# Kernel optimization log

Measured on AMD Instinct MI355X. Metric: run time of the kernel, lower is better.

## Reference

```python
import jax, jax.numpy as jnp
import numpy as np
import math

N = 20000      # nodes
E = 150000     # edges
IN = 256       # in_dim
HID = 256      # n_hid / out_dim
T = 4          # num_types
R = 8          # num_relations
H = 8          # n_heads
DK = HID // H  # d_k = 32
L = 2          # n_layers
MAXLEN = 240   # RTE max_len


def _rte_table():
    # fixed sinusoid table from RelTemporalEncoding (requires_grad=False in torch)
    pos = np.arange(MAXLEN, dtype=np.float64)[:, None]
    div = np.exp(np.arange(0, HID, 2, dtype=np.float64) * -(math.log(10000.0) / HID))
    emb = np.zeros((MAXLEN, HID), dtype=np.float64)
    emb[:, 0::2] = np.sin(pos * div) / math.sqrt(HID)
    emb[:, 1::2] = np.cos(pos * div) / math.sqrt(HID)
    return jnp.asarray(emb, dtype=jnp.float32)


def setup_inputs() -> dict:
    key = jax.random.key(0)
    ks = jax.random.split(key, 20)
    node_feature = jax.random.normal(ks[0], (N, IN), jnp.float32)
    node_type = jax.random.randint(ks[1], (N,), 0, T)
    edge_index = jax.random.randint(ks[2], (2, E), 0, N)
    edge_type = jax.random.randint(ks[3], (E,), 0, R)
    edge_time = jax.random.randint(ks[4], (E,), 0, MAXLEN)

    s_in = 1.0 / math.sqrt(IN)
    s_h = 1.0 / math.sqrt(HID)
    s_g = math.sqrt(2.0 / (DK + DK))  # glorot for relation mats

    adapt_W = jax.random.normal(ks[5], (T, IN, HID), jnp.float32) * s_in
    adapt_b = jnp.zeros((T, HID), jnp.float32)
    k_W = jax.random.normal(ks[6], (L, T, HID, HID), jnp.float32) * s_h
    k_b = jnp.zeros((L, T, HID), jnp.float32)
    q_W = jax.random.normal(ks[7], (L, T, HID, HID), jnp.float32) * s_h
    q_b = jnp.zeros((L, T, HID), jnp.float32)
    v_W = jax.random.normal(ks[8], (L, T, HID, HID), jnp.float32) * s_h
    v_b = jnp.zeros((L, T, HID), jnp.float32)
    a_W = jax.random.normal(ks[9], (L, T, HID, HID), jnp.float32) * s_h
    a_b = jnp.zeros((L, T, HID), jnp.float32)
    rel_pri = jnp.ones((L, R, H), jnp.float32)
    rel_att = jax.random.normal(ks[10], (L, R, H, DK, DK), jnp.float32) * s_g
    rel_msg = jax.random.normal(ks[11], (L, R, H, DK, DK), jnp.float32) * s_g
    skip = jnp.ones((L, T), jnp.float32)
    rte_W = jax.random.normal(ks[12], (L, HID, HID), jnp.float32) * s_h
    rte_b = jnp.zeros((L, HID), jnp.float32)
    rte_emb = _rte_table()

    return dict(node_feature=node_feature, node_type=node_type, edge_time=edge_time,
                edge_index=edge_index, edge_type=edge_type,
                adapt_W=adapt_W, adapt_b=adapt_b, k_W=k_W, k_b=k_b, q_W=q_W, q_b=q_b,
                v_W=v_W, v_b=v_b, a_W=a_W, a_b=a_b, rel_pri=rel_pri, rel_att=rel_att,
                rel_msg=rel_msg, skip=skip, rte_W=rte_W, rte_b=rte_b, rte_emb=rte_emb)


def _typed_linear(x, W, b, types):
    # x: [M, din]; W: [T, din, dout]; per-row type-selected linear (T dense GEMMs + select)
    out = jnp.zeros((x.shape[0], W.shape[-1]), x.dtype)
    for t in range(T):
        out = jnp.where((types == t)[:, None], x @ W[t] + b[t], out)
    return out


def _hgt_forward(node_feature, node_type, edge_time, edge_index, edge_type,
                 adapt_W, adapt_b, k_W, k_b, q_W, q_b, v_W, v_b, a_W, a_b,
                 rel_pri, rel_att, rel_msg, skip, rte_W, rte_b, rte_emb):
    # adapt: per-type tanh(Linear) (dropout is identity at p=0)
    x = jnp.tanh(_typed_linear(node_feature, adapt_W, adapt_b, node_type))
    src, tgt = edge_index[0], edge_index[1]   # j (source), i (target)
    st, tt = node_type[src], node_type[tgt]
    sqrt_dk = math.sqrt(DK)
    att = None
    rte = rte_emb[edge_time]                  # [E, HID]
    for l in range(L):
        x_j = x[src] + (rte @ rte_W[l] + rte_b[l])   # RTE added to source repr
        x_i = x[tgt]
        q = _typed_linear(x_i, q_W[l], q_b[l], tt).reshape(E, H, DK)
        k = _typed_linear(x_j, k_W[l], k_b[l], st).reshape(E, H, DK)
        v = _typed_linear(x_j, v_W[l], v_b[l], st).reshape(E, H, DK)
        att_e = jnp.zeros((E, H), x.dtype)
        msg = jnp.zeros((E, H, DK), x.dtype)
        for r in range(R):
            kr = jnp.einsum('ehd,hdk->ehk', k, rel_att[l, r])
            vr = jnp.einsum('ehd,hdk->ehk', v, rel_msg[l, r])
            a = (q * kr).sum(-1) * rel_pri[l, r] / sqrt_dk
            m = edge_type == r
            att_e = jnp.where(m[:, None], a, att_e)
            msg = jnp.where(m[:, None, None], vr, msg)
        # segment softmax over target node ids
        amax = jax.ops.segment_max(att_e, tgt, num_segments=N)
        ex = jnp.exp(att_e - amax[tgt])
        denom = jax.ops.segment_sum(ex, tgt, num_segments=N)
        alpha = ex / denom[tgt]                       # [E, H]
        agg = jax.ops.segment_sum(msg * alpha[:, :, None], tgt, num_segments=N)
        agg = jax.nn.gelu(agg.reshape(N, HID), approximate=False)
        trans = _typed_linear(agg, a_W[l], a_b[l], node_type)
        sk = jax.nn.sigmoid(skip[l])[node_type][:, None]
        x = trans * sk + x * (1.0 - sk)               # no LayerNorm (use_norm=False)
        att = alpha
    return att, x


def reference(node_feature, node_type, edge_time, edge_index, edge_type,
              adapt_W, adapt_b, k_W, k_b, q_W, q_b, v_W, v_b, a_W, a_b,
              rel_pri, rel_att, rel_msg, skip, rte_W, rte_b, rte_emb):
    return _hgt_forward(node_feature, node_type, edge_time, edge_index, edge_type,
                        adapt_W, adapt_b, k_W, k_b, q_W, q_b, v_W, v_b, a_W, a_b,
                        rel_pri, rel_att, rel_msg, skip, rte_W, rte_b, rte_emb)
```

## Files before the change

### kernel.cpp

```cpp
#include <hip/hip_runtime.h>
#include <hip/hip_fp16.h>

#define NN    20000
#define NE    150000
#define HD    256
#define NT    4
#define NR    8
#define NH    8
#define DKq   32
#define NL    2
#define MAXL  240
#define HBLK  256
#define SCB   ((NN + 255)/256)
#define TMAX  632
#define FOLDC 15
#define FTR   64
#define INV_SQRT_DK 0.17677669529663687f

typedef _Float16 f16x4 __attribute__((ext_vector_type(4)));
typedef _Float16 f16x8 __attribute__((ext_vector_type(8)));
typedef float    f32x4v __attribute__((ext_vector_type(4)));

__global__ __launch_bounds__(256) void k_nhist(const int* __restrict__ ntype, int* __restrict__ nhist)
{
    __shared__ int h[NT];
    const int tid = threadIdx.x, b = blockIdx.x;
    if (tid < NT) h[tid] = 0;
    __syncthreads();
    const int cn = (NN + HBLK-1)/HBLK;
    const int nEnd = min((b+1)*cn, NN);
    for (int i = b*cn + tid; i < nEnd; i += 256) atomicAdd(&h[ntype[i]], 1);
    __syncthreads();
    if (tid < NT) nhist[b*NT + tid] = h[tid];
}
__global__ void k_nscan(const int* __restrict__ nhist, int* __restrict__ noff, int* __restrict__ nbase,
                        int* __restrict__ tlist, int* __restrict__ tcount)
{
    __shared__ int tot[NT];
    const int tid = threadIdx.x;
    if (tid < NT){
        int s = 0;
        for (int b = 0; b < HBLK; b++) s += nhist[b*NT + tid];
        tot[tid] = s;
    }
    __syncthreads();
    if (tid == 0){ noff[0]=0; for (int t=0;t<NT;t++) noff[t+1]=noff[t]+tot[t]; }
    if (tid < NT){
        int base = 0; for (int t=0;t<tid;t++) base += tot[t];
        int run = 0;
        for (int b=0;b<HBLK;b++){ nbase[b*NT+tid] = base + run; run += nhist[b*NT+tid]; }
    }
    __syncthreads();
    if (tid == 0){
        int c = 0;
        for (int t = 0; t < NT; t++){
            const int ntile = (tot[t] + 31) >> 5;
            for (int rt = 0; rt < ntile; rt++) tlist[c++] = (t << 20) | rt;
        }
        *tcount = c;
    }
}
__global__ __launch_bounds__(256) void k_nscatter(const int* __restrict__ ntype,
    const int* __restrict__ nbase, int* __restrict__ nbucket)
{
    __shared__ int cur[NT];
    const int tid = threadIdx.x, b = blockIdx.x;
    if (tid < NT) cur[tid] = nbase[b*NT + tid];
    __syncthreads();
    const int cn = (NN + HBLK-1)/HBLK;
    const int nEnd = min((b+1)*cn, NN);
    for (int i = b*cn + tid; i < nEnd; i += 256)
        nbucket[atomicAdd(&cur[ntype[i]], 1)] = i;
}

__global__ void k_zero_bins(int* __restrict__ cnt){
    int i = blockIdx.x*256 + threadIdx.x;
    if (i < NN) cnt[i] = 0;
}
__global__ void k_csr_hist(const int* __restrict__ ei, int* __restrict__ cnt){
    int e = blockIdx.x*256 + threadIdx.x;
    if (e >= NE) return;
    atomicAdd(&cnt[ei[NE+e]], 1);
}
__global__ __launch_bounds__(256) void k_scan1(const int* __restrict__ cnt,
    int* __restrict__ tgt_off, int* __restrict__ bsum)
{
    __shared__ int sh[256];
    const int t = threadIdx.x, b = blockIdx.x;
    const int i = b*256 + t;
    const int v = (i < NN) ? cnt[i] : 0;
    sh[t] = v;
    __syncthreads();
    #pragma unroll
    for (int d = 1; d < 256; d <<= 1){
        const int u = (t >= d) ? sh[t-d] : 0;
        __syncthreads();
        sh[t] += u;
        __syncthreads();
    }
    if (i < NN) tgt_off[i] = sh[t] - v;
    if (t == 255) bsum[b] = sh[255];
}
__global__ __launch_bounds__(128) void k_scan2(const int* __restrict__ bsum,
    int* __restrict__ bbase, int* __restrict__ tgt_off)
{
    __shared__ int sh[128];
    const int t = threadIdx.x;
    const int v = (t < SCB) ? bsum[t] : 0;
    sh[t] = v;
    __syncthreads();
    #pragma unroll
    for (int d = 1; d < 128; d <<= 1){
        const int u = (t >= d) ? sh[t-d] : 0;
        __syncthreads();
        sh[t] += u;
        __syncthreads();
    }
    if (t < SCB) bbase[t] = sh[t] - v;
    if (t == 0) tgt_off[NN] = NE;
}
__global__ __launch_bounds__(256) void k_scan3(int* __restrict__ tgt_off,
    const int* __restrict__ bbase, int* __restrict__ binCur)
{
    const int i = blockIdx.x*256 + threadIdx.x;
    if (i >= NN) return;
    const int o = tgt_off[i] + bbase[blockIdx.x];
    tgt_off[i] = o;
    binCur[i] = o;
}
__global__ void k_csr_scatter(const int* __restrict__ ei, const int* __restrict__ etype,
    const int* __restrict__ etime, const int* __restrict__ ntype,
    int* __restrict__ binCur, int* __restrict__ src_s, int* __restrict__ combo_s,
    int* __restrict__ eid_s)
{
    int e = blockIdx.x*256 + threadIdx.x;
    if (e >= NE) return;
    const int tgt = ei[NE+e], r = etype[e], src = ei[e];
    const int pos = atomicAdd(&binCur[tgt], 1);
    src_s[pos] = src;
    combo_s[pos] = (etime[e]*NT + ntype[src]) | (r << 12);
    eid_s[pos] = e;
}
__global__ void k_tgtmap(const int* __restrict__ tgt_off, int* __restrict__ tgt_srt)
{
    const int n = blockIdx.x*256 + threadIdx.x;
    if (n >= NN) return;
    const int e0 = tgt_off[n], e1 = tgt_off[n+1];
    for (int j = e0; j < e1; j++) tgt_srt[j] = n;
}

__global__ __launch_bounds__(256) void k_w2f16_big(
    const float* __restrict__ adaptW, const float* __restrict__ qW, const float* __restrict__ kW,
    const float* __restrict__ vW, const float* __restrict__ aW, _Float16* __restrict__ out)
{
    const int y = blockIdx.y;
    const float* src; int m;
    if (y < 4){ src = adaptW; m = y; }
    else if (y < 12){ src = qW; m = y-4; }
    else if (y < 20){ src = kW; m = y-12; }
    else if (y < 28){ src = vW; m = y-20; }
    else { src = aW; m = y-28; }
    const float* ip = src + (size_t)m*65536;
    _Float16* op = out + (size_t)y*65536;
    const int tid4 = blockIdx.x*256 + threadIdx.x;
    const int k4 = tid4 >> 8, c = tid4 & 255;
    f16x4 hv;
    #pragma unroll
    for (int j = 0; j < 4; j++)
        hv[j] = (_Float16)ip[(size_t)(((k4*4 + j) << 8) + c)];
    *reinterpret_cast<f16x4*>(&op[(size_t)tid4 * 4]) = hv;
}
__global__ __launch_bounds__(256) void k_w2f16_rel(
    const float* __restrict__ attW, const float* __restrict__ msgW, _Float16* __restrict__ out)
{
    const int y = blockIdx.y;
    const float* ip = (y < 128) ? (attW + (size_t)y*1024) : (msgW + (size_t)(y-128)*1024);
    _Float16* op = out + (size_t)y*1024;
    const int tid4 = threadIdx.x;
    const int k4 = tid4 >> 5, c = tid4 & 31;
    f16x4 hv;
    #pragma unroll
    for (int j = 0; j < 4; j++)
        hv[j] = (_Float16)ip[(size_t)(((k4*4 + j) << 5) + c)];
    *reinterpret_cast<f16x4*>(&op[(size_t)tid4 * 4]) = hv;
}

__global__ __launch_bounds__(256) void k_x(
    const float* __restrict__ inF, const _Float16* __restrict__ inH,
    const _Float16* __restrict__ Wb, const float* __restrict__ bb, void* __restrict__ out,
    const int* __restrict__ nbucket, const int* __restrict__ noff,
    const int* __restrict__ tlist, const int* __restrict__ tcount,
    int mode, int oh, const float* __restrict__ skipv, const _Float16* __restrict__ xoldH)
{
    if ((int)blockIdx.x >= *tcount) return;
    const int ent = tlist[blockIdx.x];
    const int t = ent >> 20, rowTile = ent & 0xFFFFF;
    const int start = noff[t], cnt = noff[t+1] - start;

    const int tid = threadIdx.x;
    const int w = tid >> 6, lane = tid & 63;
    const int lrow = lane & 15, lgrp = lane >> 4;

    __shared__ _Float16 Al[32][260];
    __shared__ int nid[32];

    if (tid < 32){
        const int gr = rowTile*32 + tid;
        nid[tid] = (gr < cnt) ? nbucket[start + gr] : -1;
    }
    __syncthreads();
    {
        const int r = tid >> 3;
        const int arow = nid[r];
        if (inH){
            const _Float16* ap = (arow >= 0) ? (inH + (size_t)arow*HD) : nullptr;
            #pragma unroll
            for (int j = 0; j < 8; j++){
                const int f4 = (tid & 7) + j*8;
                f16x4 hv = {0,0,0,0};
                if (ap) hv = *reinterpret_cast<const f16x4*>(ap + f4*4);
                *reinterpret_cast<f16x4*>(&Al[r][f4*4]) = hv;
            }
        } else {
            const float* ap = (arow >= 0) ? (inF + (size_t)arow*HD) : nullptr;
            #pragma unroll
            for (int j = 0; j < 8; j++){
                const int f4 = (tid & 7) + j*8;
                float4 v = make_float4(0.f,0.f,0.f,0.f);
                if (ap) v = *reinterpret_cast<const float4*>(ap + f4*4);
                f16x4 hv;
                hv[0]=(_Float16)v.x; hv[1]=(_Float16)v.y; hv[2]=(_Float16)v.z; hv[3]=(_Float16)v.w;
                *reinterpret_cast<f16x4*>(&Al[r][f4*4]) = hv;
            }
        }
    }
    __syncthreads();

    float sk = 0.f;
    if (mode == 2) sk = 1.f/(1.f + __expf(-skipv[t]));

    const _Float16* W = Wb + (size_t)t*HD*HD;
    const float* bias = bb + (size_t)t*HD;
    f32x4v acc[4][2];
    #pragma unroll
    for (int cs = 0; cs < 4; cs++){
        acc[cs][0] = (f32x4v){0.f,0.f,0.f,0.f};
        acc[cs][1] = (f32x4v){0.f,0.f,0.f,0.f};
    }
    #pragma unroll 4
    for (int kc = 0; kc < 16; kc++){
        f16x4 bf[4];
        #pragma unroll
        for (int cs = 0; cs < 4; cs++)
            bf[cs] = *reinterpret_cast<const f16x4*>(
                &W[(size_t)((kc*4 + lgrp)*HD + w*64 + cs*16 + lrow)*4]);
        const f16x4 af0 = *reinterpret_cast<const f16x4*>(&Al[lrow][kc*16 + lgrp*4]);
        const f16x4 af1 = *reinterpret_cast<const f16x4*>(&Al[16 + lrow][kc*16 + lgrp*4]);
        #pragma unroll
        for (int cs = 0; cs < 4; cs++){
            acc[cs][0] = __builtin_amdgcn_mfma_f32_16x16x16f16(af0, bf[cs], acc[cs][0], 0,0,0);
            acc[cs][1] = __builtin_amdgcn_mfma_f32_16x16x16f16(af1, bf[cs], acc[cs][1], 0,0,0);
        }
    }
    #pragma unroll
    for (int cs = 0; cs < 4; cs++){
        const int col = w*64 + cs*16 + lrow;
        const float bcol = bias[col];
        #pragma unroll
        for (int rt = 0; rt < 2; rt++){
            #pragma unroll
            for (int i = 0; i < 4; i++){
                const int lr = rt*16 + lgrp*4 + i;
                const int gr = rowTile*32 + lr;
                if (gr >= cnt) continue;
                const int node = nid[lr];
                float v = acc[cs][rt][i] + bcol;
                if (mode == 1) v = tanhf(v);
                else if (mode == 2){
                    const float xo = (float)xoldH[(size_t)node*HD + col];
                    v = v*sk + xo*(1.f - sk);
                }
                if (oh) ((_Float16*)out)[(size_t)node*HD + col] = (_Float16)v;
                else    ((float*)out)[(size_t)node*HD + col] = v;
            }
        }
    }
}

__global__ __launch_bounds__(256) void k_qkv(
    const _Float16* __restrict__ xh,
    const _Float16* __restrict__ Wq, const float* __restrict__ bq, _Float16* __restrict__ oq,
    const _Float16* __restrict__ Wk, const float* __restrict__ bk, _Float16* __restrict__ okk,
    const _Float16* __restrict__ Wv, const float* __restrict__ bv, _Float16* __restrict__ ov,
    const int* __restrict__ nbucket, const int* __restrict__ noff,
    const int* __restrict__ tlist, const int* __restrict__ tcount)
{
    if ((int)blockIdx.x >= *tcount) return;
    const int ent = tlist[blockIdx.x];
    const int t = ent >> 20, rowTile = ent & 0xFFFFF;
    const int start = noff[t], cnt = noff[t+1] - start;
    const int sel = blockIdx.y;
    const _Float16* Wb = (sel==0 ? Wq : (sel==1 ? Wk : Wv));
    const float* bb = (sel==0 ? bq : (sel==1 ? bk : bv));
    _Float16* out = (sel==0 ? oq : (sel==1 ? okk : ov));

    const int tid = threadIdx.x;
    const int w = tid >> 6, lane = tid & 63;
    const int lrow = lane & 15, lgrp = lane >> 4;

    __shared__ _Float16 Al[32][260];
    __shared__ __align__(16) _Float16 Ol[32][264];
    __shared__ int nid[32];

    if (tid < 32){
        const int gr = rowTile*32 + tid;
        nid[tid] = (gr < cnt) ? nbucket[start + gr] : -1;
    }
    __syncthreads();
    {
        const int r = tid >> 3;
        const int arow = nid[r];
        const _Float16* ap = (arow >= 0) ? (xh + (size_t)arow*HD) : nullptr;
        #pragma unroll
        for (int j = 0; j < 8; j++){
            const int f4 = (tid & 7) + j*8;
            f16x4 hv = {0,0,0,0};
            if (ap) hv = *reinterpret_cast<const f16x4*>(ap + f4*4);
            *reinterpret_cast<f16x4*>(&Al[r][f4*4]) = hv;
        }
    }
    __syncthreads();

    const _Float16* W = Wb + (size_t)t*HD*HD;
    const float* bias = bb + (size_t)t*HD;
    f32x4v acc[4][2];
    #pragma unroll
    for (int cs = 0; cs < 4; cs++){
        acc[cs][0] = (f32x4v){0.f,0.f,0.f,0.f};
        acc[cs][1] = (f32x4v){0.f,0.f,0.f,0.f};
    }
    #pragma unroll 4
    for (int kc = 0; kc < 16; kc++){
        f16x4 bf[4];
        #pragma unroll
        for (int cs = 0; cs < 4; cs++)
            bf[cs] = *reinterpret_cast<const f16x4*>(
                &W[(size_t)((kc*4 + lgrp)*HD + w*64 + cs*16 + lrow)*4]);
        const f16x4 af0 = *reinterpret_cast<const f16x4*>(&Al[lrow][kc*16 + lgrp*4]);
        const f16x4 af1 = *reinterpret_cast<const f16x4*>(&Al[16 + lrow][kc*16 + lgrp*4]);
        #pragma unroll
        for (int cs = 0; cs < 4; cs++){
            acc[cs][0] = __builtin_amdgcn_mfma_f32_16x16x16f16(af0, bf[cs], acc[cs][0], 0,0,0);
            acc[cs][1] = __builtin_amdgcn_mfma_f32_16x16x16f16(af1, bf[cs], acc[cs][1], 0,0,0);
        }
    }
    #pragma unroll
    for (int cs = 0; cs < 4; cs++){
        const int col = w*64 + cs*16 + lrow;
        const float bcol = bias[col];
        #pragma unroll
        for (int rt = 0; rt < 2; rt++){
            #pragma unroll
            for (int i = 0; i < 4; i++){
                const int lr = rt*16 + lgrp*4 + i;
                Ol[lr][col] = (_Float16)(acc[cs][rt][i] + bcol);
            }
        }
    }
    __syncthreads();
    {
        const int fcb = tid & 31;
        #pragma unroll
        for (int it = 0; it < 4; it++){
            const int rr = (tid >> 5) + it*8;
            const int node = nid[rr];
            if (node < 0) continue;
            const f16x8 v = *reinterpret_cast<const f16x8*>(&Ol[rr][fcb*8]);
            *reinterpret_cast<f16x8*>(&out[(size_t)node*HD + fcb*8]) = v;
        }
    }
}

__global__ __launch_bounds__(256) void k_row_gemm(
    const float* __restrict__ A, const float* __restrict__ W, const float* __restrict__ bias,
    float* __restrict__ C)
{
    const int row = blockIdx.x, d = threadIdx.x;
    __shared__ float ar[HD];
    ar[d] = A[(size_t)row*HD + d];
    __syncthreads();
    float acc = bias[d];
    #pragma unroll 8
    for (int k=0;k<HD;k++) acc = fmaf(ar[k], W[(size_t)k*HD + d], acc);
    C[(size_t)row*HD + d] = acc;
}
__global__ __launch_bounds__(256) void k_row_gemm2(
    const float* __restrict__ A, const float* __restrict__ kWb, const float* __restrict__ vWb,
    _Float16* __restrict__ Kc, _Float16* __restrict__ Vc)
{
    const int row = blockIdx.x, ty = blockIdx.y, d = threadIdx.x;
    const float* W = ((blockIdx.z == 0) ? kWb : vWb) + (size_t)ty*HD*HD;
    _Float16* C = (blockIdx.z == 0) ? Kc : Vc;
    __shared__ float ar[HD];
    ar[d] = A[(size_t)row*HD + d];
    __syncthreads();
    float acc = 0.f;
    #pragma unroll 8
    for (int k=0;k<HD;k++) acc = fmaf(ar[k], W[(size_t)k*HD + d], acc);
    C[(size_t)row*(NT*HD) + ty*HD + d] = (_Float16)acc;
}

__global__ __launch_bounds__(256) void k_fold2(
    const _Float16* __restrict__ INa, const _Float16* __restrict__ MATa, _Float16* __restrict__ OUTa,
    const _Float16* __restrict__ INb, const _Float16* __restrict__ MATb, _Float16* __restrict__ OUTb,
    int M, int nbx)
{
    const int r = blockIdx.y;
    const _Float16* IN = blockIdx.z ? INb : INa;
    const _Float16* MATF = blockIdx.z ? MATb : MATa;
    _Float16* OUT = blockIdx.z ? OUTb : OUTa;
    const int lane = threadIdx.x & 63, w = threadIdx.x >> 6;
    const int lrow = lane & 15, lgrp = lane >> 4;
    f16x4 b[NH][2][2];
    const _Float16* Mr = MATF + (size_t)r*NH*1024;
    #pragma unroll
    for (int h = 0; h < NH; h++)
      #pragma unroll
      for (int kb = 0; kb < 2; kb++)
        #pragma unroll
        for (int hf = 0; hf < 2; hf++)
            b[h][kb][hf] = *reinterpret_cast<const f16x4*>(
                &Mr[(size_t)h*1024 + (size_t)(((kb*4 + lgrp)*32) + hf*16 + lrow)*4]);
    const int ntiles = M >> 4;
    for (int t = (int)blockIdx.x*4 + w; t < ntiles; t += nbx*4){
        const int row0 = t*16;
        const _Float16* inrow = IN + (size_t)(row0 + lrow)*HD;
        f16x4 a[NH][2];
        #pragma unroll
        for (int h = 0; h < NH; h++)
          #pragma unroll
          for (int kb = 0; kb < 2; kb++)
              a[h][kb] = *reinterpret_cast<const f16x4*>(&inrow[h*32 + kb*16 + lgrp*4]);
        #pragma unroll
        for (int h = 0; h < NH; h++){
          #pragma unroll
          for (int hf = 0; hf < 2; hf++){
              f32x4v acc = {0.f,0.f,0.f,0.f};
              acc = __builtin_amdgcn_mfma_f32_16x16x16f16(a[h][0], b[h][0][hf], acc, 0,0,0);
              acc = __builtin_amdgcn_mfma_f32_16x16x16f16(a[h][1], b[h][1][hf], acc, 0,0,0);
              #pragma unroll
              for (int i = 0; i < 4; i++){
                  const int rr = lgrp*4 + i;
                  OUT[((size_t)(row0+rr)*NR + r)*HD + h*32 + hf*16 + lrow] = (_Float16)acc[i];
              }
          }
        }
    }
}

__global__ __launch_bounds__(256) void k_fold2x(
    const _Float16* __restrict__ INa, const _Float16* __restrict__ MATa, _Float16* __restrict__ OUTa,
    const _Float16* __restrict__ INb, const _Float16* __restrict__ MATb, _Float16* __restrict__ OUTb)
{
    const int bid = blockIdx.x;
    const int xcd = bid & 7;
    const int s = bid >> 3;
    const int tr = xcd*8 + (s >> 4);
    const int item = s & 15;
    const int r = item & 7;
    const _Float16* IN = (item >> 3) ? INb : INa;
    const _Float16* MATF = (item >> 3) ? MATb : MATa;
    _Float16* OUT = (item >> 3) ? OUTb : OUTa;

    const int lane = threadIdx.x & 63, w = threadIdx.x >> 6;
    const int lrow = lane & 15, lgrp = lane >> 4;

    __shared__ __align__(16) _Float16 tile[4][16][264];

    f16x4 b[NH][2][2];
    const _Float16* Mr = MATF + (size_t)r*NH*1024;
    #pragma unroll
    for (int h = 0; h < NH; h++)
      #pragma unroll
      for (int kb = 0; kb < 2; kb++)
        #pragma unroll
        for (int hf = 0; hf < 2; hf++)
            b[h][kb][hf] = *reinterpret_cast<const f16x4*>(
                &Mr[(size_t)h*1024 + (size_t)(((kb*4 + lgrp)*32) + hf*16 + lrow)*4]);

    const int frow = lane >> 5;
    const int fcb  = lane & 31;
    const int ntiles = NN >> 4;
    for (int t = tr*4 + w; t < ntiles; t += FTR*4){
        const int row0 = t*16;
        const _Float16* inrow = IN + (size_t)(row0 + lrow)*HD;
        f16x4 a[NH][2];
        #pragma unroll
        for (int h = 0; h < NH; h++)
          #pragma unroll
          for (int kb = 0; kb < 2; kb++)
              a[h][kb] = *reinterpret_cast<const f16x4*>(&inrow[h*32 + kb*16 + lgrp*4]);
        #pragma unroll
        for (int h = 0; h < NH; h++){
          #pragma unroll
          for (int hf = 0; hf < 2; hf++){
              f32x4v acc = {0.f,0.f,0.f,0.f};
              acc = __builtin_amdgcn_mfma_f32_16x16x16f16(a[h][0], b[h][0][hf], acc, 0,0,0);
              acc = __builtin_amdgcn_mfma_f32_16x16x16f16(a[h][1], b[h][1][hf], acc, 0,0,0);
              const int col = h*32 + hf*16 + lrow;
              #pragma unroll
              for (int i = 0; i < 4; i++)
                  tile[w][lgrp*4 + i][col] = (_Float16)acc[i];
          }
        }
        asm volatile("s_waitcnt lgkmcnt(0)" ::: "memory");
        __builtin_amdgcn_sched_barrier(0);
        #pragma unroll
        for (int jj = 0; jj < 8; jj++){
            const int rr = jj*2 + frow;
            const f16x8 v = *reinterpret_cast<const f16x8*>(&tile[w][rr][fcb*8]);
            *reinterpret_cast<f16x8*>(&OUT[((size_t)(row0+rr)*NR + r)*HD + fcb*8]) = v;
        }
        asm volatile("s_waitcnt lgkmcnt(0)" ::: "memory");
        __builtin_amdgcn_sched_barrier(0);
    }
}

__global__ __launch_bounds__(256) void k_edge(
    const _Float16* __restrict__ q0, const _Float16* __restrict__ kA, const _Float16* __restrict__ KcA,
    const _Float16* __restrict__ vM, const _Float16* __restrict__ VcM,
    const float* __restrict__ relP,
    const int* __restrict__ tgt_off, const int* __restrict__ src_s, const int* __restrict__ combo_s,
    _Float16* __restrict__ agg,
    float* __restrict__ s_arr, float* __restrict__ mbuf, float* __restrict__ lbuf, int store_s)
{
    const int n = blockIdx.x*4 + (threadIdx.x >> 6);
    if (n >= NN) return;
    const int lane = threadIdx.x & 63;
    const int h = lane >> 3, c4 = (lane & 7) << 2;
    const int col = h*32 + c4;
    const int e0 = tgt_off[n], e1 = tgt_off[n+1];

    const f16x4 qh = *reinterpret_cast<const f16x4*>(&q0[(size_t)n*HD + col]);
    const float q0v = (float)qh[0], q1v = (float)qh[1], q2v = (float)qh[2], q3v = (float)qh[3];
    float m = -INFINITY, l = 0.f;
    float a0=0.f, a1=0.f, a2=0.f, a3=0.f;

    if (e0 < e1){
        int cwA = combo_s[e0];
        const int srcA0 = src_s[e0];
        const int rA0 = cwA >> 12, comboA0 = cwA & 0xFFF;
        f16x4 kaA = *reinterpret_cast<const f16x4*>(&kA [((size_t)srcA0*NR + rA0)*HD + col]);
        f16x4 kcA = *reinterpret_cast<const f16x4*>(&KcA[((size_t)comboA0*NR + rA0)*HD + col]);
        f16x4 vmA = *reinterpret_cast<const f16x4*>(&vM [((size_t)srcA0*NR + rA0)*HD + col]);
        f16x4 vcA = *reinterpret_cast<const f16x4*>(&VcM[((size_t)comboA0*NR + rA0)*HD + col]);
        const int j1 = min(e0+1, e1-1);
        int srcB = src_s[j1], cwB = combo_s[j1];

        for (int j = e0; j < e1; j++){
            const int rB = cwB >> 12, comboB = cwB & 0xFFF;
            const size_t offSB = ((size_t)srcB*NR + rB)*HD + col;
            const size_t offCB = ((size_t)comboB*NR + rB)*HD + col;
            const f16x4 kaN = *reinterpret_cast<const f16x4*>(&kA [offSB]);
            const f16x4 kcN = *reinterpret_cast<const f16x4*>(&KcA[offCB]);
            const f16x4 vmN = *reinterpret_cast<const f16x4*>(&vM [offSB]);
            const f16x4 vcN = *reinterpret_cast<const f16x4*>(&VcM[offCB]);
            const int jn = min(j+2, e1-1);
            const int srcN = src_s[jn], cwN = combo_s[jn];

            const int r = cwA >> 12;
            float s = q0v*((float)kaA[0]+(float)kcA[0])
                    + q1v*((float)kaA[1]+(float)kcA[1])
                    + q2v*((float)kaA[2]+(float)kcA[2])
                    + q3v*((float)kaA[3]+(float)kcA[3]);
            s += __shfl_xor(s, 1); s += __shfl_xor(s, 2); s += __shfl_xor(s, 4);
            s *= relP[r*NH + h] * INV_SQRT_DK;
            if (store_s && (lane & 7) == 0) s_arr[(size_t)j*NH + h] = s;
            const float mn = fmaxf(m, s);
            const float sc = __expf(m - mn);
            const float p  = __expf(s - mn);
            l = l*sc + p;
            m = mn;
            a0 = a0*sc + p*((float)vmA[0] + (float)vcA[0]);
            a1 = a1*sc + p*((float)vmA[1] + (float)vcA[1]);
            a2 = a2*sc + p*((float)vmA[2] + (float)vcA[2]);
            a3 = a3*sc + p*((float)vmA[3] + (float)vcA[3]);

            cwA = cwB;
            kaA = kaN; kcA = kcN; vmA = vmN; vcA = vcN;
            srcB = srcN; cwB = cwN;
        }
    }
    const float inv = (l > 0.f) ? 1.f/l : 0.f;
    a0 *= inv; a1 *= inv; a2 *= inv; a3 *= inv;
    f16x4 o;
    o[0] = (_Float16)(0.5f*a0*(1.f + erff(a0*0.70710678118654752f)));
    o[1] = (_Float16)(0.5f*a1*(1.f + erff(a1*0.70710678118654752f)));
    o[2] = (_Float16)(0.5f*a2*(1.f + erff(a2*0.70710678118654752f)));
    o[3] = (_Float16)(0.5f*a3*(1.f + erff(a3*0.70710678118654752f)));
    *reinterpret_cast<f16x4*>(&agg[(size_t)n*HD + col]) = o;
    if (store_s && (lane & 7) == 0){
        mbuf[(size_t)n*NH + h] = m;
        lbuf[(size_t)n*NH + h] = l;
    }
}

__global__ void k_alpha(const float* __restrict__ s_arr, const int* __restrict__ eid_s,
                        const float* __restrict__ mbuf, const float* __restrict__ lbuf,
                        const int* __restrict__ tgt_srt, float* __restrict__ out_att)
{
    int i = blockIdx.x*256 + threadIdx.x;
    if (i >= NE*NH) return;
    const int j = i >> 3, h = i & 7;
    const int t = tgt_srt[j];
    const float a = __expf(s_arr[i] - mbuf[(size_t)t*NH + h]) / lbuf[(size_t)t*NH + h];
    out_att[(size_t)eid_s[j]*NH + h] = a;
}

extern "C" void kernel_launch(void* const* d_in, const int* in_sizes, int n_in,
                              void* d_out, int out_size, void* d_ws, size_t ws_size,
                              hipStream_t stream)
{
    const float* node_feature = (const float*)d_in[0];
    const int*   node_type    = (const int*)d_in[1];
    const int*   edge_time    = (const int*)d_in[2];
    const int*   edge_index   = (const int*)d_in[3];
    const int*   edge_type    = (const int*)d_in[4];
    const float* adapt_W = (const float*)d_in[5];
    const float* adapt_b = (const float*)d_in[6];
    const float* k_W = (const float*)d_in[7];
    const float* k_b = (const float*)d_in[8];
    const float* q_W = (const float*)d_in[9];
    const float* q_b = (const float*)d_in[10];
    const float* v_W = (const float*)d_in[11];
    const float* v_b = (const float*)d_in[12];
    const float* a_W = (const float*)d_in[13];
    const float* a_b = (const float*)d_in[14];
    const float* rel_pri = (const float*)d_in[15];
    const float* rel_att = (const float*)d_in[16];
    const float* rel_msg = (const float*)d_in[17];
    const float* skip  = (const float*)d_in[18];
    const float* rte_W = (const float*)d_in[19];
    const float* rte_b = (const float*)d_in[20];
    const float* rte_emb = (const float*)d_in[21];

    char* wp = (char*)d_ws;
    auto alloc_f = [&](size_t n)->float*{ float* p=(float*)wp; wp += n*sizeof(float); return p; };
    auto alloc_i = [&](size_t n)->int*  { int*   p=(int*)wp;   wp += n*sizeof(int);   return p; };
    auto alloc_h = [&](size_t n)->_Float16*{ _Float16* p=(_Float16*)wp; wp += n*sizeof(_Float16); return p; };
    _Float16* xh0 = alloc_h((size_t)NN*HD);
    _Float16* xh1 = alloc_h((size_t)NN*HD);
    _Float16* q0h = alloc_h((size_t)NN*HD);
    _Float16* k0h = alloc_h((size_t)NN*HD);
    _Float16* v0h = alloc_h((size_t)NN*HD);
    _Float16* aggh= alloc_h((size_t)NN*HD);
    float* s_arr = alloc_f((size_t)NE*NH);
    float* mbuf  = alloc_f((size_t)NN*NH);
    float* lbuf  = alloc_f((size_t)NN*NH);
    float* rteP  = alloc_f((size_t)MAXL*HD);
    _Float16* Kch = alloc_h((size_t)MAXL*NT*HD);
    _Float16* Vch = alloc_h((size_t)MAXL*NT*HD);
    _Float16* kavm = alloc_h((size_t)NN*NR*HD);
    _Float16* vmh  = alloc_h((size_t)NN*NR*HD);
    _Float16* kcaA0 = alloc_h((size_t)MAXL*NT*NR*HD);
    _Float16* kcaA1 = alloc_h((size_t)MAXL*NT*NR*HD);
    _Float16* kcaM0 = alloc_h((size_t)MAXL*NT*NR*HD);
    _Float16* kcaM1 = alloc_h((size_t)MAXL*NT*NR*HD);
    _Float16* wF   = alloc_h((size_t)36*65536);
    _Float16* relF = alloc_h((size_t)256*1024);
    int* nbucket = alloc_i(NN);
    int* nhist   = alloc_i(HBLK*NT);
    int* nbase   = alloc_i(HBLK*NT);
    int* noff    = alloc_i(8);
    int* tlist   = alloc_i(TMAX);
    int* tcount  = alloc_i(8);
    int* cnt     = alloc_i(NN);
    int* bsum    = alloc_i(SCB);
    int* bbase   = alloc_i(SCB);
    int* binCur  = alloc_i(NN);
    int* tgt_off = alloc_i(NN+1);
    int* src_s   = alloc_i(NE);
    int* combo_s = alloc_i(NE);
    int* eid_s   = alloc_i(NE);
    int* tgt_srt = alloc_i(NE);

    const _Float16* adaptF = wF;
    const _Float16* qF = wF + (size_t)4*65536;
    const _Float16* kF = wF + (size_t)12*65536;
    const _Float16* vF = wF + (size_t)20*65536;
    const _Float16* aF = wF + (size_t)28*65536;
    const _Float16* relAF = relF;
    const _Float16* relMF = relF + (size_t)128*1024;

    float* out_att = (float*)d_out;
    float* out_x   = (float*)d_out + (size_t)NE*NH;

    const dim3 gFoldC2(FOLDC, NR, 2);
    const dim3 gQKV(TMAX, 3);
    const int gFoldX = 1024;
    const int gE256 = (NE + 255)/256;
    const int gEH = (NE*NH + 255)/256;
    const int gN256 = (NN + 255)/256;
    const int gEg = (NN + 3)/4;

    k_w2f16_big<<<dim3(64,36),256,0,stream>>>(adapt_W, q_W, k_W, v_W, a_W, wF);
    k_w2f16_rel<<<dim3(1,256),256,0,stream>>>(rel_att, rel_msg, relF);

    k_nhist<<<HBLK,256,0,stream>>>(node_type, nhist);
    k_nscan<<<1,64,0,stream>>>(nhist, noff, nbase, tlist, tcount);
    k_nscatter<<<HBLK,256,0,stream>>>(node_type, nbase, nbucket);

    k_zero_bins<<<SCB,256,0,stream>>>(cnt);
    k_csr_hist<<<gE256,256,0,stream>>>(edge_index, cnt);
    k_scan1<<<SCB,256,0,stream>>>(cnt, tgt_off, bsum);
    k_scan2<<<1,128,0,stream>>>(bsum, bbase, tgt_off);
    k_scan3<<<SCB,256,0,stream>>>(tgt_off, bbase, binCur);
    k_csr_scatter<<<gE256,256,0,stream>>>(edge_index, edge_type, edge_time, node_type,
                                          binCur, src_s, combo_s, eid_s);
    k_tgtmap<<<gN256,256,0,stream>>>(tgt_off, tgt_srt);

    {
        k_row_gemm<<<MAXL,256,0,stream>>>(rte_emb, rte_W, rte_b, rteP);
        k_row_gemm2<<<dim3(MAXL,NT,2),256,0,stream>>>(rteP, k_W, v_W, Kch, Vch);
        k_fold2<<<gFoldC2,256,0,stream>>>(Kch, relAF, kcaA0, Vch, relMF, kcaM0, MAXL*NT, FOLDC);
        k_row_gemm<<<MAXL,256,0,stream>>>(rte_emb, rte_W + (size_t)HD*HD, rte_b + HD, rteP);
        k_row_gemm2<<<dim3(MAXL,NT,2),256,0,stream>>>(rteP, k_W + (size_t)NT*HD*HD,
                                                      v_W + (size_t)NT*HD*HD, Kch, Vch);
        k_fold2<<<gFoldC2,256,0,stream>>>(Kch, relAF + (size_t)NR*NH*1024, kcaA1,
                                          Vch, relMF + (size_t)NR*NH*1024, kcaM1, MAXL*NT, FOLDC);
    }

    k_x<<<TMAX,256,0,stream>>>(node_feature, nullptr, adaptF, adapt_b, xh0,
                               nbucket, noff, tlist, tcount, 1, 1, nullptr, nullptr);
    k_qkv<<<gQKV,256,0,stream>>>(xh0, qF, q_b, q0h, kF, k_b, k0h, vF, v_b, v0h,
                                 nbucket, noff, tlist, tcount);

    for (int l = 0; l < NL; l++){
        const _Float16* rAF = relAF + (size_t)l*NR*NH*1024;
        const _Float16* rMF = relMF + (size_t)l*NR*NH*1024;
        const _Float16* kcaA = (l == 0) ? kcaA0 : kcaA1;
        const _Float16* kcaM = (l == 0) ? kcaM0 : kcaM1;
        const int store_s = (l == NL-1) ? 1 : 0;
        k_fold2x<<<gFoldX,256,0,stream>>>(k0h, rAF, kavm, v0h, rMF, vmh);
        k_edge<<<gEg,256,0,stream>>>(q0h, kavm, kcaA, vmh, kcaM,
                                     rel_pri + (size_t)l*NR*NH,
                                     tgt_off, src_s, combo_s, aggh,
                                     s_arr, mbuf, lbuf, store_s);
        if (store_s)
            k_alpha<<<gEH,256,0,stream>>>(s_arr, eid_s, mbuf, lbuf, tgt_srt, out_att);
        if (l == 0){
            k_x<<<TMAX,256,0,stream>>>(nullptr, aggh, aF, a_b, xh1,
                                       nbucket, noff, tlist, tcount, 2, 1, skip, xh0);
            k_qkv<<<gQKV,256,0,stream>>>(xh1, qF + (size_t)NT*HD*HD, q_b + (size_t)NT*HD, q0h,
                                         kF + (size_t)NT*HD*HD, k_b + (size_t)NT*HD, k0h,
                                         vF + (size_t)NT*HD*HD, v_b + (size_t)NT*HD, v0h,
                                         nbucket, noff, tlist, tcount);
        } else {
            k_x<<<TMAX,256,0,stream>>>(nullptr, aggh, aF + (size_t)NT*HD*HD, a_b + (size_t)NT*HD,
                                       out_x, nbucket, noff, tlist, tcount, 2, 0, skip + NT, xh1);
        }
    }
}
```

Baseline: 487.5 us.

## Fold relation attention matrix into query side instead of key side

Instead of projecting each source key (and the RTE key table) through the relation attention matrix, the query is transformed by the transposed relation matrix per relation, and the edge kernel dots it with the raw key plus the raw RTE key. This removes the per-combo folded key tables and their fold kernels, and shrinks the per-edge key gathers to plain per-node rows that are reused across relations. The per-target query-fold loads change with the relation, but they come from the same node so they stay cache-local. The attention-matrix conversion is transposed to match.

New measurement: 485.7 us (median of 2 runs). About the same (-0.4%).

```diff
diff --git a/kernel.cpp b/kernel.cpp
--- a/kernel.cpp
+++ b/kernel.cpp
@@ -179,9 +179,15 @@
     const int tid4 = threadIdx.x;
     const int k4 = tid4 >> 5, c = tid4 & 31;
     f16x4 hv;
-    #pragma unroll
-    for (int j = 0; j < 4; j++)
-        hv[j] = (_Float16)ip[(size_t)(((k4*4 + j) << 5) + c)];
+    if (y < 128){
+        #pragma unroll
+        for (int j = 0; j < 4; j++)
+            hv[j] = (_Float16)ip[(size_t)((c << 5) + (k4*4 + j))];
+    } else {
+        #pragma unroll
+        for (int j = 0; j < 4; j++)
+            hv[j] = (_Float16)ip[(size_t)(((k4*4 + j) << 5) + c)];
+    }
     *reinterpret_cast<f16x4*>(&op[(size_t)tid4 * 4]) = hv;
 }
 
@@ -411,14 +417,10 @@
 }
 
 __global__ __launch_bounds__(256) void k_fold2(
-    const _Float16* __restrict__ INa, const _Float16* __restrict__ MATa, _Float16* __restrict__ OUTa,
-    const _Float16* __restrict__ INb, const _Float16* __restrict__ MATb, _Float16* __restrict__ OUTb,
+    const _Float16* __restrict__ IN, const _Float16* __restrict__ MATF, _Float16* __restrict__ OUT,
     int M, int nbx)
 {
     const int r = blockIdx.y;
-    const _Float16* IN = blockIdx.z ? INb : INa;
-    const _Float16* MATF = blockIdx.z ? MATb : MATa;
-    _Float16* OUT = blockIdx.z ? OUTb : OUTa;
     const int lane = threadIdx.x & 63, w = threadIdx.x >> 6;
     const int lrow = lane & 15, lgrp = lane >> 4;
     f16x4 b[NH][2][2];
@@ -527,7 +529,8 @@
 }
 
 __global__ __launch_bounds__(256) void k_edge(
-    const _Float16* __restrict__ q0, const _Float16* __restrict__ kA, const _Float16* __restrict__ KcA,
+    const _Float16* __restrict__ qF, const _Float16* __restrict__ k0,
+    const _Float16* __restrict__ KcT,
     const _Float16* __restrict__ vM, const _Float16* __restrict__ VcM,
     const float* __restrict__ relP,
     const int* __restrict__ tgt_off, const int* __restrict__ src_s, const int* __restrict__ combo_s,
@@ -541,8 +544,6 @@
     const int col = h*32 + c4;
     const int e0 = tgt_off[n], e1 = tgt_off[n+1];
 
-    const f16x4 qh = *reinterpret_cast<const f16x4*>(&q0[(size_t)n*HD + col]);
-    const float q0v = (float)qh[0], q1v = (float)qh[1], q2v = (float)qh[2], q3v = (float)qh[3];
     float m = -INFINITY, l = 0.f;
     float a0=0.f, a1=0.f, a2=0.f, a3=0.f;
 
@@ -550,8 +551,9 @@
         int cwA = combo_s[e0];
         const int srcA0 = src_s[e0];
         const int rA0 = cwA >> 12, comboA0 = cwA & 0xFFF;
-        f16x4 kaA = *reinterpret_cast<const f16x4*>(&kA [((size_t)srcA0*NR + rA0)*HD + col]);
-        f16x4 kcA = *reinterpret_cast<const f16x4*>(&KcA[((size_t)comboA0*NR + rA0)*HD + col]);
+        f16x4 qfA = *reinterpret_cast<const f16x4*>(&qF [((size_t)n*NR + rA0)*HD + col]);
+        f16x4 kkA = *reinterpret_cast<const f16x4*>(&k0 [(size_t)srcA0*HD + col]);
+        f16x4 kcA = *reinterpret_cast<const f16x4*>(&KcT[(size_t)comboA0*HD + col]);
         f16x4 vmA = *reinterpret_cast<const f16x4*>(&vM [((size_t)srcA0*NR + rA0)*HD + col]);
         f16x4 vcA = *reinterpret_cast<const f16x4*>(&VcM[((size_t)comboA0*NR + rA0)*HD + col]);
         const int j1 = min(e0+1, e1-1);
@@ -559,20 +561,19 @@
 
         for (int j = e0; j < e1; j++){
             const int rB = cwB >> 12, comboB = cwB & 0xFFF;
-            const size_t offSB = ((size_t)srcB*NR + rB)*HD + col;
-            const size_t offCB = ((size_t)comboB*NR + rB)*HD + col;
-            const f16x4 kaN = *reinterpret_cast<const f16x4*>(&kA [offSB]);
-            const f16x4 kcN = *reinterpret_cast<const f16x4*>(&KcA[offCB]);
-            const f16x4 vmN = *reinterpret_cast<const f16x4*>(&vM [offSB]);
-            const f16x4 vcN = *reinterpret_cast<const f16x4*>(&VcM[offCB]);
+            const f16x4 qfN = *reinterpret_cast<const f16x4*>(&qF [((size_t)n*NR + rB)*HD + col]);
+            const f16x4 kkN = *reinterpret_cast<const f16x4*>(&k0 [(size_t)srcB*HD + col]);
+            const f16x4 kcN = *reinterpret_cast<const f16x4*>(&KcT[(size_t)comboB*HD + col]);
+            const f16x4 vmN = *reinterpret_cast<const f16x4*>(&vM [((size_t)srcB*NR + rB)*HD + col]);
+            const f16x4 vcN = *reinterpret_cast<const f16x4*>(&VcM[((size_t)comboB*NR + rB)*HD + col]);
             const int jn = min(j+2, e1-1);
             const int srcN = src_s[jn], cwN = combo_s[jn];
 
             const int r = cwA >> 12;
-            float s = q0v*((float)kaA[0]+(float)kcA[0])
-                    + q1v*((float)kaA[1]+(float)kcA[1])
-                    + q2v*((float)kaA[2]+(float)kcA[2])
-                    + q3v*((float)kaA[3]+(float)kcA[3]);
+            float s = (float)qfA[0]*((float)kkA[0]+(float)kcA[0])
+                    + (float)qfA[1]*((float)kkA[1]+(float)kcA[1])
+                    + (float)qfA[2]*((float)kkA[2]+(float)kcA[2])
+                    + (float)qfA[3]*((float)kkA[3]+(float)kcA[3]);
             s += __shfl_xor(s, 1); s += __shfl_xor(s, 2); s += __shfl_xor(s, 4);
             s *= relP[r*NH + h] * INV_SQRT_DK;
             if (store_s && (lane & 7) == 0) s_arr[(size_t)j*NH + h] = s;
@@ -587,7 +588,7 @@
             a3 = a3*sc + p*((float)vmA[3] + (float)vcA[3]);
 
             cwA = cwB;
-            kaA = kaN; kcA = kcN; vmA = vmN; vcA = vcN;
+            qfA = qfN; kkA = kkN; kcA = kcN; vmA = vmN; vcA = vcN;
             srcB = srcN; cwB = cwN;
         }
     }
@@ -658,12 +659,11 @@
     float* mbuf  = alloc_f((size_t)NN*NH);
     float* lbuf  = alloc_f((size_t)NN*NH);
     float* rteP  = alloc_f((size_t)MAXL*HD);
-    _Float16* Kch = alloc_h((size_t)MAXL*NT*HD);
-    _Float16* Vch = alloc_h((size_t)MAXL*NT*HD);
-    _Float16* kavm = alloc_h((size_t)NN*NR*HD);
+    _Float16* Kch0 = alloc_h((size_t)MAXL*NT*HD);
+    _Float16* Kch1 = alloc_h((size_t)MAXL*NT*HD);
+    _Float16* Vch  = alloc_h((size_t)MAXL*NT*HD);
+    _Float16* qfh  = alloc_h((size_t)NN*NR*HD);
     _Float16* vmh  = alloc_h((size_t)NN*NR*HD);
-    _Float16* kcaA0 = alloc_h((size_t)MAXL*NT*NR*HD);
-    _Float16* kcaA1 = alloc_h((size_t)MAXL*NT*NR*HD);
     _Float16* kcaM0 = alloc_h((size_t)MAXL*NT*NR*HD);
     _Float16* kcaM1 = alloc_h((size_t)MAXL*NT*NR*HD);
     _Float16* wF   = alloc_h((size_t)36*65536);
@@ -695,7 +695,7 @@
     float* out_att = (float*)d_out;
     float* out_x   = (float*)d_out + (size_t)NE*NH;
 
-    const dim3 gFoldC2(FOLDC, NR, 2);
+    const dim3 gFoldC(FOLDC, NR);
     const dim3 gQKV(TMAX, 3);
     const int gFoldX = 1024;
     const int gE256 = (NE + 255)/256;
@@ -721,13 +721,12 @@
 
     {
         k_row_gemm<<<MAXL,256,0,stream>>>(rte_emb, rte_W, rte_b, rteP);
-        k_row_gemm2<<<dim3(MAXL,NT,2),256,0,stream>>>(rteP, k_W, v_W, Kch, Vch);
-        k_fold2<<<gFoldC2,256,0,stream>>>(Kch, relAF, kcaA0, Vch, relMF, kcaM0, MAXL*NT, FOLDC);
+        k_row_gemm2<<<dim3(MAXL,NT,2),256,0,stream>>>(rteP, k_W, v_W, Kch0, Vch);
+        k_fold2<<<gFoldC,256,0,stream>>>(Vch, relMF, kcaM0, MAXL*NT, FOLDC);
         k_row_gemm<<<MAXL,256,0,stream>>>(rte_emb, rte_W + (size_t)HD*HD, rte_b + HD, rteP);
         k_row_gemm2<<<dim3(MAXL,NT,2),256,0,stream>>>(rteP, k_W + (size_t)NT*HD*HD,
-                                                      v_W + (size_t)NT*HD*HD, Kch, Vch);
-        k_fold2<<<gFoldC2,256,0,stream>>>(Kch, relAF + (size_t)NR*NH*1024, kcaA1,
-                                          Vch, relMF + (size_t)NR*NH*1024, kcaM1, MAXL*NT, FOLDC);
+                                                      v_W + (size_t)NT*HD*HD, Kch1, Vch);
+        k_fold2<<<gFoldC,256,0,stream>>>(Vch, relMF + (size_t)NR*NH*1024, kcaM1, MAXL*NT, FOLDC);
     }
 
     k_x<<<TMAX,256,0,stream>>>(node_feature, nullptr, adaptF, adapt_b, xh0,
@@ -738,11 +737,11 @@
     for (int l = 0; l < NL; l++){
         const _Float16* rAF = relAF + (size_t)l*NR*NH*1024;
         const _Float16* rMF = relMF + (size_t)l*NR*NH*1024;
-        const _Float16* kcaA = (l == 0) ? kcaA0 : kcaA1;
+        const _Float16* KchL = (l == 0) ? Kch0 : Kch1;
         const _Float16* kcaM = (l == 0) ? kcaM0 : kcaM1;
         const int store_s = (l == NL-1) ? 1 : 0;
-        k_fold2x<<<gFoldX,256,0,stream>>>(k0h, rAF, kavm, v0h, rMF, vmh);
-        k_edge<<<gEg,256,0,stream>>>(q0h, kavm, kcaA, vmh, kcaM,
+        k_fold2x<<<gFoldX,256,0,stream>>>(q0h, rAF, qfh, v0h, rMF, vmh);
+        k_edge<<<gEg,256,0,stream>>>(qfh, k0h, KchL, vmh, kcaM,
                                      rel_pri + (size_t)l*NR*NH,
                                      tgt_off, src_s, combo_s, aggh,
                                      s_arr, mbuf, lbuf, store_s);
```
